# Kernel optimization log

Hardware: AMD Instinct MI355X
Metric: run time of the kernel (lower is better)

The kernel has to match this reference:

```python
import jax, jax.numpy as jnp
import numpy as np

B, T, N, D = 4, 4, 256, 128  # batch, time_steps, num_nodes, features (in==out)
EPS = 1e-5
NEG = -1e9


def _glorot(key, shape):
    fan_in, fan_out = shape[0], shape[1]
    s = float(np.sqrt(6.0 / (fan_in + fan_out)))
    return jax.random.uniform(key, shape, jnp.float32, -s, s)


def setup_inputs() -> dict:
    key = jax.random.key(0)
    ks = jax.random.split(key, 8)
    x = jax.random.normal(ks[0], (B, T, N, D), jnp.float32)
    adj = (jax.random.uniform(ks[1], (N, N)) < 0.05).astype(jnp.float32)
    adj = jnp.maximum(adj, jnp.eye(N, dtype=jnp.float32))
    weight = _glorot(ks[2], (D, D))            # GCN weight [in, out]
    bias = jnp.zeros((D,), jnp.float32)
    att_w1 = _glorot(ks[3], (2 * D, D))        # Linear(2D -> D), column layout
    att_b1 = jnp.zeros((D,), jnp.float32)
    att_w2 = _glorot(ks[4], (D, 1))            # Linear(D -> 1)
    att_b2 = jnp.zeros((1,), jnp.float32)
    ln_gamma = jnp.ones((D,), jnp.float32)
    ln_beta = jnp.zeros((D,), jnp.float32)
    return dict(x=x, adj_matrix=adj, weight=weight, bias=bias,
                att_w1=att_w1, att_b1=att_b1, att_w2=att_w2, att_b2=att_b2,
                ln_gamma=ln_gamma, ln_beta=ln_beta)


def _layer_norm(y, gamma, beta):
    mu = jnp.mean(y, axis=-1, keepdims=True)
    var = jnp.mean(jnp.square(y - mu), axis=-1, keepdims=True)
    return (y - mu) * jax.lax.rsqrt(var + EPS) * gamma + beta


def reference(x, adj_matrix, weight, bias, att_w1, att_b1, att_w2, att_b2,
              ln_gamma, ln_beta):
    d_out = weight.shape[1]
    # split the first attention Linear so cat([h_i, h_j]) @ W1 == h_i@W1a + h_j@W1b
    W1a, W1b = att_w1[:d_out], att_w1[d_out:]
    w2 = att_w2[:, 0]
    mask = adj_matrix[None] == 0  # [1, N, N]

    def step(carry, x_t):  # x_t: [B, N, D]
        h = x_t @ weight + bias                                  # [B, N, D]
        a = h @ W1a                                              # [B, N, D]
        b = h @ W1b                                              # [B, N, D]
        # big intermediate the kernel would fuse away: [B, N, N, D]
        e = jax.nn.leaky_relu(a[:, :, None, :] + b[:, None, :, :] + att_b1, 0.2)
        scores = jnp.einsum('bijd,d->bij', e, w2) + att_b2[0]    # [B, N, N]
        scores = jnp.where(mask, NEG, scores)
        attn = jax.nn.softmax(scores, axis=-1)  # dropout is identity in eval
        agg = jnp.einsum('bij,bjd->bid', attn, h)                # [B, N, D]
        out = _layer_norm(agg + x_t, ln_gamma, ln_beta)          # in==out residual
        return carry, out

    _, ys = jax.lax.scan(step, None, jnp.swapaxes(x, 0, 1))      # [T, B, N, D]
    return jax.nn.relu(jnp.swapaxes(ys, 0, 1))                   # [B, T, N, D]
```

## Files before the change

### kernel.cpp

```cpp
#include <hip/hip_runtime.h>
#include <hip/hip_bf16.h>

#define BT 16
#define NN 256
#define DD 128
#define MROWS (BT*NN)

typedef __bf16 bf16x8 __attribute__((ext_vector_type(8)));
typedef float  f32x4  __attribute__((ext_vector_type(4)));

#define LREL(z) ((z) >= 0.0f ? (z) : 0.2f * (z))
#define HS_STRIDE 136

__global__ __launch_bounds__(256) void gemm2_kernel(
        const float* __restrict__ x, const float* __restrict__ weight,
        const float* __restrict__ bias, const float* __restrict__ attw1,
        const float* __restrict__ attb1,
        float* __restrict__ hbuf, float* __restrict__ abuf,
        float* __restrict__ bbuf) {
    int tid = threadIdx.x;
    int w = tid >> 6, l = tid & 63;
    int row0 = blockIdx.x * 16;
    int lrow = l & 15, lk8 = (l >> 4) * 8;

    __shared__ __align__(16) __bf16 hs[16][HS_STRIDE];

    const float* abase = x + (size_t)(row0 + lrow) * DD + lk8;
    bf16x8 af[4];
#pragma unroll
    for (int kt = 0; kt < 4; ++kt) {
        float4 u0 = *(const float4*)(abase + 32 * kt);
        float4 u1 = *(const float4*)(abase + 32 * kt + 4);
        af[kt][0]=(__bf16)u0.x; af[kt][1]=(__bf16)u0.y;
        af[kt][2]=(__bf16)u0.z; af[kt][3]=(__bf16)u0.w;
        af[kt][4]=(__bf16)u1.x; af[kt][5]=(__bf16)u1.y;
        af[kt][6]=(__bf16)u1.z; af[kt][7]=(__bf16)u1.w;
    }

#pragma unroll
    for (int s = 0; s < 2; ++s) {
        int n0 = (w + 4 * s) * 16;
        int ncol = n0 + lrow;
        bf16x8 wf[4];
#pragma unroll
        for (int kt = 0; kt < 4; ++kt) {
            const float* wp = weight + (size_t)(lk8 + 32 * kt) * DD + ncol;
#pragma unroll
            for (int j = 0; j < 8; ++j)
                wf[kt][j] = (__bf16)wp[(size_t)j * DD];
        }
        f32x4 acc = {0.f, 0.f, 0.f, 0.f};
        acc = __builtin_amdgcn_mfma_f32_16x16x32_bf16(af[0], wf[0], acc, 0, 0, 0);
        acc = __builtin_amdgcn_mfma_f32_16x16x32_bf16(af[1], wf[1], acc, 0, 0, 0);
        acc = __builtin_amdgcn_mfma_f32_16x16x32_bf16(af[2], wf[2], acc, 0, 0, 0);
        acc = __builtin_amdgcn_mfma_f32_16x16x32_bf16(af[3], wf[3], acc, 0, 0, 0);

        float bb = bias[ncol];
        int rloc = (l >> 4) * 4;
        float* hout = hbuf + (size_t)(row0 + rloc) * DD + ncol;
#pragma unroll
        for (int r = 0; r < 4; ++r) {
            float hv = acc[r] + bb;
            hout[(size_t)r * DD] = hv;
            hs[rloc + r][ncol] = (__bf16)hv;
        }
    }
    __syncthreads();

    bf16x8 ha[4];
#pragma unroll
    for (int kt = 0; kt < 4; ++kt)
        ha[kt] = *(const bf16x8*)(&hs[lrow][lk8 + 32 * kt]);

#pragma unroll
    for (int h2 = 0; h2 < 2; ++h2) {
#pragma unroll
        for (int s = 0; s < 2; ++s) {
            int n0 = (w + 4 * s) * 16;
            int ncol = n0 + lrow;
            bf16x8 w1f[4];
#pragma unroll
            for (int kt = 0; kt < 4; ++kt) {
                const float* wp = attw1 + (size_t)(h2 * DD + lk8 + 32 * kt) * DD + ncol;
#pragma unroll
                for (int j = 0; j < 8; ++j)
                    w1f[kt][j] = (__bf16)wp[(size_t)j * DD];
            }
            f32x4 acc = {0.f, 0.f, 0.f, 0.f};
            acc = __builtin_amdgcn_mfma_f32_16x16x32_bf16(ha[0], w1f[0], acc, 0, 0, 0);
            acc = __builtin_amdgcn_mfma_f32_16x16x32_bf16(ha[1], w1f[1], acc, 0, 0, 0);
            acc = __builtin_amdgcn_mfma_f32_16x16x32_bf16(ha[2], w1f[2], acc, 0, 0, 0);
            acc = __builtin_amdgcn_mfma_f32_16x16x32_bf16(ha[3], w1f[3], acc, 0, 0, 0);

            float bb = h2 ? attb1[ncol] : 0.f;
            float* dst = (h2 ? bbuf : abuf) + (size_t)(row0 + (l >> 4) * 4) * DD + ncol;
#pragma unroll
            for (int r = 0; r < 4; ++r)
                dst[(size_t)r * DD] = acc[r] + bb;
        }
    }
}

__global__ __launch_bounds__(256) void attn_kernel(
        const float* __restrict__ hbuf, const float* __restrict__ abuf,
        const float* __restrict__ bbuf, const float* __restrict__ x,
        const float* __restrict__ adj, const float* __restrict__ w2,
        const float* __restrict__ gamma, const float* __restrict__ beta,
        float* __restrict__ out) {
    int tid = threadIdx.x;
    int w = tid >> 6, l = tid & 63;
    int i  = (blockIdx.x & 63) * 4 + w;
    int bt = blockIdx.x >> 6;

    __shared__ int nbr_l[4][64];

    int cnt = 0;
    const float* adjrow = adj + (size_t)i * NN;
    for (int jt = 0; jt < NN / 64; ++jt) {
        int j = jt * 64 + l;
        float v = adjrow[j];
        unsigned long long mask = __ballot(v != 0.f);
        if (v != 0.f) {
            int pos = cnt + __popcll(mask & ((1ull << l) - 1ull));
            if (pos < 64) nbr_l[w][pos] = j;
        }
        cnt += __popcll(mask);
    }
    cnt = min(cnt, 64);
    int jreg = nbr_l[w][l];

    const float* arow = abuf + (size_t)(bt * NN + i) * DD;
    float a0 = arow[l], a1 = arow[l + 64];
    float w20 = w2[l],  w21 = w2[l + 64];
    const float* bbase = bbuf + (size_t)bt * NN * DD;

    float m = -3.0e38f, myp = 0.f;
    int c = 0;
    for (; c + 3 < cnt; c += 4) {
        int j0 = __shfl(jreg, c);
        int j1 = __shfl(jreg, c + 1);
        int j2 = __shfl(jreg, c + 2);
        int j3 = __shfl(jreg, c + 3);
        const float* B0 = bbase + (size_t)j0 * DD;
        const float* B1 = bbase + (size_t)j1 * DD;
        const float* B2 = bbase + (size_t)j2 * DD;
        const float* B3 = bbase + (size_t)j3 * DD;
        float p0 = LREL(a0 + B0[l]) * w20 + LREL(a1 + B0[l + 64]) * w21;
        float p1 = LREL(a0 + B1[l]) * w20 + LREL(a1 + B1[l + 64]) * w21;
        float p2 = LREL(a0 + B2[l]) * w20 + LREL(a1 + B2[l + 64]) * w21;
        float p3 = LREL(a0 + B3[l]) * w20 + LREL(a1 + B3[l + 64]) * w21;
#pragma unroll
        for (int off = 32; off; off >>= 1) {
            p0 += __shfl_xor(p0, off);
            p1 += __shfl_xor(p1, off);
            p2 += __shfl_xor(p2, off);
            p3 += __shfl_xor(p3, off);
        }
        myp = (l == c)     ? p0 : myp;
        myp = (l == c + 1) ? p1 : myp;
        myp = (l == c + 2) ? p2 : myp;
        myp = (l == c + 3) ? p3 : myp;
        m = fmaxf(m, fmaxf(fmaxf(p0, p1), fmaxf(p2, p3)));
    }
    for (; c < cnt; ++c) {
        int j0 = __shfl(jreg, c);
        const float* B0 = bbase + (size_t)j0 * DD;
        float p0 = LREL(a0 + B0[l]) * w20 + LREL(a1 + B0[l + 64]) * w21;
#pragma unroll
        for (int off = 32; off; off >>= 1) p0 += __shfl_xor(p0, off);
        myp = (l == c) ? p0 : myp;
        m = fmaxf(m, p0);
    }

    float wgt = (l < cnt) ? __expf(myp - m) : 0.f;
    float dsum = wgt;
#pragma unroll
    for (int off = 32; off; off >>= 1) dsum += __shfl_xor(dsum, off);
    float inv = 1.f / dsum;

    const float* hbase = hbuf + (size_t)bt * NN * DD;
    float acc0 = 0.f, acc1 = 0.f;
    c = 0;
    for (; c + 3 < cnt; c += 4) {
        float wc0 = __shfl(wgt, c),     wc1 = __shfl(wgt, c + 1);
        float wc2 = __shfl(wgt, c + 2), wc3 = __shfl(wgt, c + 3);
        int j0 = __shfl(jreg, c),     j1 = __shfl(jreg, c + 1);
        int j2 = __shfl(jreg, c + 2), j3 = __shfl(jreg, c + 3);
        const float* H0 = hbase + (size_t)j0 * DD;
        const float* H1 = hbase + (size_t)j1 * DD;
        const float* H2 = hbase + (size_t)j2 * DD;
        const float* H3 = hbase + (size_t)j3 * DD;
        acc0 += wc0 * H0[l]      + wc1 * H1[l]      + wc2 * H2[l]      + wc3 * H3[l];
        acc1 += wc0 * H0[l + 64] + wc1 * H1[l + 64] + wc2 * H2[l + 64] + wc3 * H3[l + 64];
    }
    for (; c < cnt; ++c) {
        float wc = __shfl(wgt, c);
        int j = __shfl(jreg, c);
        const float* H = hbase + (size_t)j * DD;
        acc0 += wc * H[l];
        acc1 += wc * H[l + 64];
    }

    const float* xrow = x + (size_t)(bt * NN + i) * DD;
    float y0 = acc0 * inv + xrow[l];
    float y1 = acc1 * inv + xrow[l + 64];

    float s = y0 + y1;
#pragma unroll
    for (int off = 32; off; off >>= 1) s += __shfl_xor(s, off);
    float mu = s * (1.0f / 128.0f);
    float v0 = y0 - mu, v1 = y1 - mu;
    float vs = v0 * v0 + v1 * v1;
#pragma unroll
    for (int off = 32; off; off >>= 1) vs += __shfl_xor(vs, off);
    float rstd = rsqrtf(vs * (1.0f / 128.0f) + 1e-5f);

    float o0 = v0 * rstd * gamma[l]      + beta[l];
    float o1 = v1 * rstd * gamma[l + 64] + beta[l + 64];

    float* orow = out + (size_t)(bt * NN + i) * DD;
    orow[l]      = fmaxf(o0, 0.0f);
    orow[l + 64] = fmaxf(o1, 0.0f);
}

extern "C" void kernel_launch(void* const* d_in, const int* in_sizes, int n_in,
                              void* d_out, int out_size, void* d_ws, size_t ws_size,
                              hipStream_t stream) {
    const float* x      = (const float*)d_in[0];
    const float* adj    = (const float*)d_in[1];
    const float* weight = (const float*)d_in[2];
    const float* bias   = (const float*)d_in[3];
    const float* attw1  = (const float*)d_in[4];
    const float* attb1  = (const float*)d_in[5];
    const float* attw2  = (const float*)d_in[6];
    const float* gamma  = (const float*)d_in[8];
    const float* beta   = (const float*)d_in[9];
    float* out = (float*)d_out;

    char* p = (char*)d_ws;
    float* hbuf = (float*)p;          p += (size_t)MROWS * DD * 4;
    float* abuf = (float*)p;          p += (size_t)MROWS * DD * 4;
    float* bbuf = (float*)p;

    gemm2_kernel<<<MROWS / 16, 256, 0, stream>>>(x, weight, bias, attw1, attb1,
                                                 hbuf, abuf, bbuf);
    attn_kernel<<<NN / 4 * BT, 256, 0, stream>>>(hbuf, abuf, bbuf, x, adj,
                                                 attw2, gamma, beta, out);
}
```

Baseline: 28.35 us.

## Store h/a/b intermediates as bf16 and split GEMM blocks by attention half

The intermediate buffers h, a and b are now stored in bf16 instead of fp32, halving workspace traffic for both the write in the GEMM kernel and the gathered neighbor reads in the attention kernel. The GEMM grid is doubled: each block pair recomputes h for the same 16 rows, and then one block computes a and the other computes b, which adds parallelism at the cost of computing the first GEMM twice. Storing a, b and h in bf16 lowers intermediate precision, which may affect accuracy.

Measured after the change: 26.97 us. 1.05x faster.

```diff
diff --git a/kernel.cpp b/kernel.cpp
--- a/kernel.cpp
+++ b/kernel.cpp
@@ -16,11 +16,12 @@
         const float* __restrict__ x, const float* __restrict__ weight,
         const float* __restrict__ bias, const float* __restrict__ attw1,
         const float* __restrict__ attb1,
-        float* __restrict__ hbuf, float* __restrict__ abuf,
-        float* __restrict__ bbuf) {
+        __bf16* __restrict__ hbuf, __bf16* __restrict__ abuf,
+        __bf16* __restrict__ bbuf) {
     int tid = threadIdx.x;
     int w = tid >> 6, l = tid & 63;
-    int row0 = blockIdx.x * 16;
+    int chunk = blockIdx.x >> 1, parity = blockIdx.x & 1;
+    int row0 = chunk * 16;
     int lrow = l & 15, lk8 = (l >> 4) * 8;
 
     __shared__ __align__(16) __bf16 hs[16][HS_STRIDE];
@@ -57,12 +58,12 @@
 
         float bb = bias[ncol];
         int rloc = (l >> 4) * 4;
-        float* hout = hbuf + (size_t)(row0 + rloc) * DD + ncol;
+        __bf16* hout = hbuf + (size_t)(row0 + rloc) * DD + ncol;
 #pragma unroll
         for (int r = 0; r < 4; ++r) {
-            float hv = acc[r] + bb;
-            hout[(size_t)r * DD] = hv;
-            hs[rloc + r][ncol] = (__bf16)hv;
+            __bf16 hv = (__bf16)(acc[r] + bb);
+            hs[rloc + r][ncol] = hv;
+            if (parity == 0) hout[(size_t)r * DD] = hv;
         }
     }
     __syncthreads();
@@ -73,37 +74,34 @@
         ha[kt] = *(const bf16x8*)(&hs[lrow][lk8 + 32 * kt]);
 
 #pragma unroll
-    for (int h2 = 0; h2 < 2; ++h2) {
-#pragma unroll
-        for (int s = 0; s < 2; ++s) {
-            int n0 = (w + 4 * s) * 16;
-            int ncol = n0 + lrow;
-            bf16x8 w1f[4];
-#pragma unroll
-            for (int kt = 0; kt < 4; ++kt) {
-                const float* wp = attw1 + (size_t)(h2 * DD + lk8 + 32 * kt) * DD + ncol;
-#pragma unroll
-                for (int j = 0; j < 8; ++j)
-                    w1f[kt][j] = (__bf16)wp[(size_t)j * DD];
-            }
-            f32x4 acc = {0.f, 0.f, 0.f, 0.f};
-            acc = __builtin_amdgcn_mfma_f32_16x16x32_bf16(ha[0], w1f[0], acc, 0, 0, 0);
-            acc = __builtin_amdgcn_mfma_f32_16x16x32_bf16(ha[1], w1f[1], acc, 0, 0, 0);
-            acc = __builtin_amdgcn_mfma_f32_16x16x32_bf16(ha[2], w1f[2], acc, 0, 0, 0);
-            acc = __builtin_amdgcn_mfma_f32_16x16x32_bf16(ha[3], w1f[3], acc, 0, 0, 0);
-
-            float bb = h2 ? attb1[ncol] : 0.f;
-            float* dst = (h2 ? bbuf : abuf) + (size_t)(row0 + (l >> 4) * 4) * DD + ncol;
-#pragma unroll
-            for (int r = 0; r < 4; ++r)
-                dst[(size_t)r * DD] = acc[r] + bb;
-        }
+    for (int s = 0; s < 2; ++s) {
+        int n0 = (w + 4 * s) * 16;
+        int ncol = n0 + lrow;
+        bf16x8 w1f[4];
+#pragma unroll
+        for (int kt = 0; kt < 4; ++kt) {
+            const float* wp = attw1 + (size_t)(parity * DD + lk8 + 32 * kt) * DD + ncol;
+#pragma unroll
+            for (int j = 0; j < 8; ++j)
+                w1f[kt][j] = (__bf16)wp[(size_t)j * DD];
+        }
+        f32x4 acc = {0.f, 0.f, 0.f, 0.f};
+        acc = __builtin_amdgcn_mfma_f32_16x16x32_bf16(ha[0], w1f[0], acc, 0, 0, 0);
+        acc = __builtin_amdgcn_mfma_f32_16x16x32_bf16(ha[1], w1f[1], acc, 0, 0, 0);
+        acc = __builtin_amdgcn_mfma_f32_16x16x32_bf16(ha[2], w1f[2], acc, 0, 0, 0);
+        acc = __builtin_amdgcn_mfma_f32_16x16x32_bf16(ha[3], w1f[3], acc, 0, 0, 0);
+
+        float bb = parity ? attb1[ncol] : 0.f;
+        __bf16* dst = (parity ? bbuf : abuf) + (size_t)(row0 + (l >> 4) * 4) * DD + ncol;
+#pragma unroll
+        for (int r = 0; r < 4; ++r)
+            dst[(size_t)r * DD] = (__bf16)(acc[r] + bb);
     }
 }
 
 __global__ __launch_bounds__(256) void attn_kernel(
-        const float* __restrict__ hbuf, const float* __restrict__ abuf,
-        const float* __restrict__ bbuf, const float* __restrict__ x,
+        const __bf16* __restrict__ hbuf, const __bf16* __restrict__ abuf,
+        const __bf16* __restrict__ bbuf, const float* __restrict__ x,
         const float* __restrict__ adj, const float* __restrict__ w2,
         const float* __restrict__ gamma, const float* __restrict__ beta,
         float* __restrict__ out) {
@@ -129,10 +127,10 @@
     cnt = min(cnt, 64);
     int jreg = nbr_l[w][l];
 
-    const float* arow = abuf + (size_t)(bt * NN + i) * DD;
-    float a0 = arow[l], a1 = arow[l + 64];
+    const __bf16* arow = abuf + (size_t)(bt * NN + i) * DD;
+    float a0 = (float)arow[l], a1 = (float)arow[l + 64];
     float w20 = w2[l],  w21 = w2[l + 64];
-    const float* bbase = bbuf + (size_t)bt * NN * DD;
+    const __bf16* bbase = bbuf + (size_t)bt * NN * DD;
 
     float m = -3.0e38f, myp = 0.f;
     int c = 0;
@@ -141,14 +139,14 @@
         int j1 = __shfl(jreg, c + 1);
         int j2 = __shfl(jreg, c + 2);
         int j3 = __shfl(jreg, c + 3);
-        const float* B0 = bbase + (size_t)j0 * DD;
-        const float* B1 = bbase + (size_t)j1 * DD;
-        const float* B2 = bbase + (size_t)j2 * DD;
-        const float* B3 = bbase + (size_t)j3 * DD;
-        float p0 = LREL(a0 + B0[l]) * w20 + LREL(a1 + B0[l + 64]) * w21;
-        float p1 = LREL(a0 + B1[l]) * w20 + LREL(a1 + B1[l + 64]) * w21;
-        float p2 = LREL(a0 + B2[l]) * w20 + LREL(a1 + B2[l + 64]) * w21;
-        float p3 = LREL(a0 + B3[l]) * w20 + LREL(a1 + B3[l + 64]) * w21;
+        const __bf16* B0 = bbase + (size_t)j0 * DD;
+        const __bf16* B1 = bbase + (size_t)j1 * DD;
+        const __bf16* B2 = bbase + (size_t)j2 * DD;
+        const __bf16* B3 = bbase + (size_t)j3 * DD;
+        float p0 = LREL(a0 + (float)B0[l]) * w20 + LREL(a1 + (float)B0[l + 64]) * w21;
+        float p1 = LREL(a0 + (float)B1[l]) * w20 + LREL(a1 + (float)B1[l + 64]) * w21;
+        float p2 = LREL(a0 + (float)B2[l]) * w20 + LREL(a1 + (float)B2[l + 64]) * w21;
+        float p3 = LREL(a0 + (float)B3[l]) * w20 + LREL(a1 + (float)B3[l + 64]) * w21;
 #pragma unroll
         for (int off = 32; off; off >>= 1) {
             p0 += __shfl_xor(p0, off);
@@ -164,8 +162,8 @@
     }
     for (; c < cnt; ++c) {
         int j0 = __shfl(jreg, c);
-        const float* B0 = bbase + (size_t)j0 * DD;
-        float p0 = LREL(a0 + B0[l]) * w20 + LREL(a1 + B0[l + 64]) * w21;
+        const __bf16* B0 = bbase + (size_t)j0 * DD;
+        float p0 = LREL(a0 + (float)B0[l]) * w20 + LREL(a1 + (float)B0[l + 64]) * w21;
 #pragma unroll
         for (int off = 32; off; off >>= 1) p0 += __shfl_xor(p0, off);
         myp = (l == c) ? p0 : myp;
@@ -178,7 +176,7 @@
     for (int off = 32; off; off >>= 1) dsum += __shfl_xor(dsum, off);
     float inv = 1.f / dsum;
 
-    const float* hbase = hbuf + (size_t)bt * NN * DD;
+    const __bf16* hbase = hbuf + (size_t)bt * NN * DD;
     float acc0 = 0.f, acc1 = 0.f;
     c = 0;
     for (; c + 3 < cnt; c += 4) {
@@ -186,19 +184,21 @@
         float wc2 = __shfl(wgt, c + 2), wc3 = __shfl(wgt, c + 3);
         int j0 = __shfl(jreg, c),     j1 = __shfl(jreg, c + 1);
         int j2 = __shfl(jreg, c + 2), j3 = __shfl(jreg, c + 3);
-        const float* H0 = hbase + (size_t)j0 * DD;
-        const float* H1 = hbase + (size_t)j1 * DD;
-        const float* H2 = hbase + (size_t)j2 * DD;
-        const float* H3 = hbase + (size_t)j3 * DD;
-        acc0 += wc0 * H0[l]      + wc1 * H1[l]      + wc2 * H2[l]      + wc3 * H3[l];
-        acc1 += wc0 * H0[l + 64] + wc1 * H1[l + 64] + wc2 * H2[l + 64] + wc3 * H3[l + 64];
+        const __bf16* H0 = hbase + (size_t)j0 * DD;
+        const __bf16* H1 = hbase + (size_t)j1 * DD;
+        const __bf16* H2 = hbase + (size_t)j2 * DD;
+        const __bf16* H3 = hbase + (size_t)j3 * DD;
+        acc0 += wc0 * (float)H0[l]      + wc1 * (float)H1[l]
+              + wc2 * (float)H2[l]      + wc3 * (float)H3[l];
+        acc1 += wc0 * (float)H0[l + 64] + wc1 * (float)H1[l + 64]
+              + wc2 * (float)H2[l + 64] + wc3 * (float)H3[l + 64];
     }
     for (; c < cnt; ++c) {
         float wc = __shfl(wgt, c);
         int j = __shfl(jreg, c);
-        const float* H = hbase + (size_t)j * DD;
-        acc0 += wc * H[l];
-        acc1 += wc * H[l + 64];
+        const __bf16* H = hbase + (size_t)j * DD;
+        acc0 += wc * (float)H[l];
+        acc1 += wc * (float)H[l + 64];
     }
 
     const float* xrow = x + (size_t)(bt * NN + i) * DD;
@@ -238,12 +238,12 @@
     float* out = (float*)d_out;
 
     char* p = (char*)d_ws;
-    float* hbuf = (float*)p;          p += (size_t)MROWS * DD * 4;
-    float* abuf = (float*)p;          p += (size_t)MROWS * DD * 4;
-    float* bbuf = (float*)p;
-
-    gemm2_kernel<<<MROWS / 16, 256, 0, stream>>>(x, weight, bias, attw1, attb1,
-                                                 hbuf, abuf, bbuf);
+    __bf16* hbuf = (__bf16*)p;        p += (size_t)MROWS * DD * 2;
+    __bf16* abuf = (__bf16*)p;        p += (size_t)MROWS * DD * 2;
+    __bf16* bbuf = (__bf16*)p;
+
+    gemm2_kernel<<<MROWS / 16 * 2, 256, 0, stream>>>(x, weight, bias, attw1, attb1,
+                                                     hbuf, abuf, bbuf);
     attn_kernel<<<NN / 4 * BT, 256, 0, stream>>>(hbuf, abuf, bbuf, x, adj,
                                                  attw2, gamma, beta, out);
 }
```
